# Optimization experiments

Measured on AMD Instinct MI355X. Metric: run time of the kernel, lower is better.

The kernel has to match this reference:

```python
import jax, jax.numpy as jnp
import numpy as np

N, K, M, C, OUT, S = 80000, 8, 1000, 128, 64, 2
EPS = 1e-5


def _bn(x, g, b, m, v):
    # eval-mode BatchNorm1d applied over the last (channel) axis
    return (x - m) * (g / jnp.sqrt(v + EPS)) + b


def setup_inputs() -> dict:
    key = jax.random.key(0)
    ks = jax.random.split(key, 40)
    it = iter(range(40))
    rn = lambda sh, s=1.0: jax.random.normal(ks[next(it)], sh, dtype=jnp.float32) * s
    ru = lambda sh: jax.random.uniform(ks[next(it)], sh, dtype=jnp.float32, minval=0.5, maxval=1.5)
    w = 0.05
    inp = {}
    inp["sp_fea"] = rn((M, C))
    inp["sp_xyz"] = rn((M, 3))
    inp["o_p_fea"] = rn((N, C))
    inp["p_xyz"] = rn((N, 3))
    # linear_q / linear_k / linear_v  (in_planes -> mid_planes)
    inp["Wq"] = rn((C, C), w); inp["bq"] = jnp.zeros((C,), jnp.float32)
    inp["Wk"] = rn((C, C), w); inp["bk"] = jnp.zeros((C,), jnp.float32)
    inp["Wv"] = rn((C, C), w); inp["bv"] = jnp.zeros((C,), jnp.float32)
    # linear_p: Linear(3,3) -> BN(3) -> ReLU -> Linear(3, mid)
    inp["Wp1"] = rn((3, 3), 0.5); inp["bp1"] = jnp.zeros((3,), jnp.float32)
    inp["gp"] = 1.0 + rn((3,), 0.1); inp["betap"] = rn((3,), 0.1)
    inp["mp"] = rn((3,), 0.1); inp["vp"] = ru((3,))
    inp["Wp2"] = rn((3, C), 0.3); inp["bp2"] = jnp.zeros((C,), jnp.float32)
    # linear_w: BN(mid) -> ReLU -> Linear(mid,out) -> BN(out) -> ReLU -> Linear(out,out)
    inp["g1"] = 1.0 + rn((C,), 0.1); inp["beta1"] = rn((C,), 0.1)
    inp["m1"] = rn((C,), 0.1); inp["v1"] = ru((C,))
    inp["W1"] = rn((C, OUT), w); inp["b1"] = jnp.zeros((OUT,), jnp.float32)
    inp["g2"] = 1.0 + rn((OUT,), 0.1); inp["beta2"] = rn((OUT,), 0.1)
    inp["m2"] = rn((OUT,), 0.1); inp["v2"] = ru((OUT,))
    inp["W2"] = rn((OUT, OUT), w); inp["b2"] = jnp.zeros((OUT,), jnp.float32)
    # index / offset inputs (ints)
    inp["c2p_idx_abs"] = jax.random.randint(ks[next(it)], (N, K), 0, M)
    inp["c2p_idx"] = jax.random.randint(ks[next(it)], (N, K), 0, M)
    inp["cluster_idx"] = jax.random.randint(ks[next(it)], (N,), 0, M)
    inp["offset"] = jnp.array([N], dtype=jnp.int32)
    inp["sp_offset"] = jnp.array([M], dtype=jnp.int32)
    return inp


def reference(sp_fea, sp_xyz, o_p_fea, p_xyz,
              Wq, bq, Wk, bk, Wv, bv,
              Wp1, bp1, gp, betap, mp, vp, Wp2, bp2,
              g1, beta1, m1, v1, W1, b1,
              g2, beta2, m2, v2, W2, b2,
              c2p_idx_abs, c2p_idx, cluster_idx, offset, sp_offset):
    q = o_p_fea @ Wq + bq                               # [N, C]
    k_sp = (sp_fea @ Wk + bk)[c2p_idx_abs]              # gather -> [N, K, C]
    v_sp = (sp_fea @ Wv + bv)[c2p_idx_abs]              # [N, K, C]
    p_e = sp_xyz[c2p_idx_abs]                           # [N, K, 3]
    # positional encoding MLP
    p_e = jax.nn.relu(_bn(p_e @ Wp1 + bp1, gp, betap, mp, vp)) @ Wp2 + bp2  # [N, K, C]
    # vector attention scores
    w = k_sp - q[:, None, :] + p_e                      # [N, K, C]
    w = jax.nn.relu(_bn(w, g1, beta1, m1, v1)) @ W1 + b1
    w = jax.nn.relu(_bn(w, g2, beta2, m2, v2)) @ W2 + b2  # [N, K, OUT]
    w = jax.nn.softmax(w, axis=1)                        # softmax over the K neighbors
    # shared-plane weighted sum
    bi = ((v_sp + p_e).reshape(N, K, S, C // S) * w[:, :, None, :]).reshape(N, K, C)
    bi = bi.sum(axis=2)                                  # [N, K]
    return jax.nn.softmax(bi, axis=1)                    # association matrix [N, K]
```

## Files before the change

### kernel.cpp

```cpp
#include <hip/hip_runtime.h>
#include <stdint.h>

#define EPS 1e-5f
#define LOG2E 1.4426950408889634f

#define NPTS 80000
#define CDIM 128
#define ODIM 64
#define KNBR 8
#define MSUP 1000

#define KP2H_OFF 0
#define UT_OFF   (256*1024)
#define WQF_OFF  (512*1024)
#define W1F_OFF  (544*1024)
#define W2F_OFF  (560*1024)
#define C1_OFF   (568*1024)
#define QSG_OFF  (576*1024)
#define WSTAGE_BYTES (16*1024 + 8*1024 + 256)

typedef float f32x4 __attribute__((ext_vector_type(4)));
typedef short bf16x8 __attribute__((ext_vector_type(8)));
typedef __bf16 bf16v8 __attribute__((ext_vector_type(8)));
typedef __bf16 bf16v4 __attribute__((ext_vector_type(4)));

union FragU { bf16x8 v; unsigned u[4]; uint4 q; };

#if __has_builtin(__builtin_amdgcn_cvt_pk_bf16_f32)
#define HAVE_PK_BF16 1
#endif

__device__ inline unsigned pk_bf16(float lo, float hi) {
#ifdef HAVE_PK_BF16
  typedef __bf16 bf16x2_t __attribute__((ext_vector_type(2)));
  return __builtin_bit_cast(unsigned, __builtin_amdgcn_cvt_pk_bf16_f32(lo, hi));
#else
  unsigned a = __builtin_bit_cast(unsigned, lo);
  unsigned b = __builtin_bit_cast(unsigned, hi);
  a += 0x7FFFu + ((a >> 16) & 1u);
  b += 0x7FFFu + ((b >> 16) & 1u);
  return (a >> 16) | (b & 0xFFFF0000u);
#endif
}

__device__ inline float exp2_fast(float x) {
#if __has_builtin(__builtin_amdgcn_exp2f)
  return __builtin_amdgcn_exp2f(x);
#else
  return exp2f(x);
#endif
}

__global__ __launch_bounds__(256)
void k_prep(const float* __restrict__ sp_fea, const float* __restrict__ sp_xyz,
            const float* __restrict__ Wk, const float* __restrict__ bk,
            const float* __restrict__ Wv, const float* __restrict__ bv,
            const float* __restrict__ Wp1, const float* __restrict__ bp1,
            const float* __restrict__ gp, const float* __restrict__ betap,
            const float* __restrict__ mp, const float* __restrict__ vp,
            const float* __restrict__ Wp2, const float* __restrict__ bp2,
            const float* __restrict__ g1, const float* __restrict__ beta1,
            const float* __restrict__ m1, const float* __restrict__ v1,
            const float* __restrict__ bq,
            const float* __restrict__ Wq, const float* __restrict__ W1,
            const float* __restrict__ W2,
            const float* __restrict__ g2, const float* __restrict__ v2,
            const float* __restrict__ b1, const float* __restrict__ m2,
            const float* __restrict__ beta2, char* __restrict__ ws)
{
  if (blockIdx.x < 1000) {
    unsigned short* kp2h = (unsigned short*)(ws + KP2H_OFF);
    float* uT = (float*)(ws + UT_OFF);
    const int m = blockIdx.x;
    const int t = threadIdx.x;
    const int c = t & 127, half = t >> 7;
    __shared__ float fea[128];
    __shared__ float pk[128], pv[128];
    if (t < 128) fea[t] = sp_fea[m * 128 + t];
    __syncthreads();
    float kv = 0.f, vv = 0.f;
    const float* wkc = Wk + half * 64 * 128 + c;
    const float* wvc = Wv + half * 64 * 128 + c;
    const float* feah = fea + half * 64;
    #pragma unroll 8
    for (int d = 0; d < 64; ++d) {
      const float f = feah[d];
      kv = fmaf(f, wkc[d * 128], kv);
      vv = fmaf(f, wvc[d * 128], vv);
    }
    if (half) { pk[c] = kv; pv[c] = vv; }
    __syncthreads();
    if (!half) {
      kv += pk[c] + bk[c];
      vv += pv[c] + bv[c];
      const float x0 = sp_xyz[m*3+0], x1 = sp_xyz[m*3+1], x2 = sp_xyz[m*3+2];
      float pe = bp2[c];
      #pragma unroll
      for (int ii = 0; ii < 3; ++ii) {
        float s = bp1[ii] + x0*Wp1[0*3+ii] + x1*Wp1[1*3+ii] + x2*Wp1[2*3+ii];
        s = (s - mp[ii]) * (gp[ii] * rsqrtf(vp[ii] + EPS)) + betap[ii];
        s = fmaxf(s, 0.0f);
        pe += s * Wp2[ii*128 + c];
      }
      const float s1c = g1[c] * rsqrtf(v1[c] + EPS);
      const float kpv = (kv + pe - m1[c] - bq[c]) * s1c + beta1[c];
      kp2h[m*128 + c] = (unsigned short)(pk_bf16(kpv, kpv) & 0xFFFFu);
      pv[c] = vv + pe;
    }
    __syncthreads();
    if (t < 64) uT[m*64 + t] = (pv[t] + pv[t + 64]) * LOG2E;
  } else {
    const int tid = (blockIdx.x - 1000) * 256 + threadIdx.x;
    if (tid < 2048) {
      const int e = tid, f = e >> 6, l = e & 63;
      const int kt = f >> 3, mt = f & 7;
      const int c = mt*16 + (l & 15);
      const int d0 = kt*32 + (l >> 4)*8;
      const float sc = g1[c] * rsqrtf(v1[c] + EPS);
      uint4 u;
      u.x = pk_bf16(Wq[(d0+0)*128 + c]*sc, Wq[(d0+1)*128 + c]*sc);
      u.y = pk_bf16(Wq[(d0+2)*128 + c]*sc, Wq[(d0+3)*128 + c]*sc);
      u.z = pk_bf16(Wq[(d0+4)*128 + c]*sc, Wq[(d0+5)*128 + c]*sc);
      u.w = pk_bf16(Wq[(d0+6)*128 + c]*sc, Wq[(d0+7)*128 + c]*sc);
      *(uint4*)(ws + WQF_OFF + e*16) = u;
    } else if (tid < 3072) {
      const int e = tid - 2048, f = e >> 6, l = e & 63;
      const int kt = f >> 2, jt = f & 3;
      const int j = jt*16 + (l & 15);
      const int c0 = kt*32 + (l >> 4)*8;
      const float sc = g2[j] * rsqrtf(v2[j] + EPS);
      uint4 u;
      u.x = pk_bf16(W1[(c0+0)*64 + j]*sc, W1[(c0+1)*64 + j]*sc);
      u.y = pk_bf16(W1[(c0+2)*64 + j]*sc, W1[(c0+3)*64 + j]*sc);
      u.z = pk_bf16(W1[(c0+4)*64 + j]*sc, W1[(c0+5)*64 + j]*sc);
      u.w = pk_bf16(W1[(c0+6)*64 + j]*sc, W1[(c0+7)*64 + j]*sc);
      *(uint4*)(ws + W1F_OFF + e*16) = u;
    } else if (tid < 3584) {
      const int e = tid - 3072, f = e >> 6, l = e & 63;
      const int kt2 = f >> 2, nt = f & 3;
      const int jp = nt*16 + (l & 15);
      const int j0 = kt2*32 + (l >> 4)*8;
      uint4 u;
      u.x = pk_bf16(W2[(j0+0)*64 + jp]*LOG2E, W2[(j0+1)*64 + jp]*LOG2E);
      u.y = pk_bf16(W2[(j0+2)*64 + jp]*LOG2E, W2[(j0+3)*64 + jp]*LOG2E);
      u.z = pk_bf16(W2[(j0+4)*64 + jp]*LOG2E, W2[(j0+5)*64 + jp]*LOG2E);
      u.w = pk_bf16(W2[(j0+6)*64 + jp]*LOG2E, W2[(j0+7)*64 + jp]*LOG2E);
      *(uint4*)(ws + W2F_OFF + e*16) = u;
    } else if (tid < 3648) {
      const int j = tid - 3584;
      const float sc = g2[j] * rsqrtf(v2[j] + EPS);
      ((float*)(ws + C1_OFF))[j] = (b1[j] - m2[j]) * sc + beta2[j];
    }
  }
}

__global__ __launch_bounds__(256, 4)
void k_q(const float* __restrict__ o_p_fea, char* __restrict__ ws)
{
  __shared__ __align__(16) char ldsq[32*1024];
  char* qs_g = ws + QSG_OFF;
  const int t = threadIdx.x;
  const int wave = t >> 6, l = t & 63;
  const int quad = l >> 4, row = l & 15;
  const int n0 = (blockIdx.x * 4 + wave) * 16;

  {
    const uint4* src = (const uint4*)(ws + WQF_OFF);
    uint4* dst = (uint4*)ldsq;
    #pragma unroll
    for (int i = 0; i < 8; ++i) dst[t + i*256] = src[t + i*256];
  }
  __syncthreads();

  f32x4 qa[8];
  #pragma unroll
  for (int mt = 0; mt < 8; ++mt) qa[mt] = (f32x4){0.f, 0.f, 0.f, 0.f};
  const float* feab = o_p_fea + (size_t)(n0 + row) * 128;
  #pragma unroll
  for (int kt = 0; kt < 4; ++kt) {
    f32x4 fa = *(const f32x4*)(feab + kt*32 + quad*8);
    f32x4 fb = *(const f32x4*)(feab + kt*32 + quad*8 + 4);
    FragU bu;
    bu.u[0] = pk_bf16(fa[0], fa[1]);
    bu.u[1] = pk_bf16(fa[2], fa[3]);
    bu.u[2] = pk_bf16(fb[0], fb[1]);
    bu.u[3] = pk_bf16(fb[2], fb[3]);
    #pragma unroll
    for (int mt = 0; mt < 8; ++mt) {
      const bf16x8 wf = *(const bf16x8*)(ldsq + ((kt*8+mt)*64 + l)*16);
      qa[mt] = __builtin_amdgcn_mfma_f32_16x16x32_bf16(wf, bu.v, qa[mt], 0, 0, 0);
    }
  }
  #pragma unroll
  for (int mt = 0; mt < 8; ++mt) {
    uint2 pp;
    pp.x = pk_bf16(qa[mt][0], qa[mt][1]);
    pp.y = pk_bf16(qa[mt][2], qa[mt][3]);
    *(uint2*)(qs_g + (size_t)(n0 + row) * 256 + mt*32 + quad*8) = pp;
  }
}

#define H2_PITCH 144
#define H2_SIZE  (16*144)
#define W1L_OFF  0
#define W2L_OFF  (16*1024)
#define C1L_OFF  (24*1024)
#define H2_BASE  24832
#define LDS_TOTAL (H2_BASE + 4*H2_SIZE)

__global__ __launch_bounds__(256, 3)
void k_main(const int* __restrict__ idx, const float* __restrict__ b2,
            const char* __restrict__ ws, float* __restrict__ out)
{
  const unsigned short* kp2h = (const unsigned short*)(ws + KP2H_OFF);
  const float* uT = (const float*)(ws + UT_OFF);
  const char* qs_g = ws + QSG_OFF;

  __shared__ __align__(16) char lds[LDS_TOTAL];
  const int t = threadIdx.x;
  const int wave = t >> 6, l = t & 63;
  const int quad = l >> 4, row = l & 15;
  char* h2_w = lds + H2_BASE + wave * H2_SIZE;

  const int slot = blockIdx.x * 4 + wave;
  const int gid0 = slot * 4;
  const int nloc = row >> 3;

  {
    const uint4* src = (const uint4*)(ws + W1F_OFF);
    uint4* dst = (uint4*)lds;
    #pragma unroll
    for (int i = 0; i < 7; ++i) {
      const int e = t + i * 256;
      if (e < WSTAGE_BYTES / 16) dst[e] = src[e];
    }
  }

  int mr4[4];
  #pragma unroll
  for (int g = 0; g < 4; ++g) mr4[g] = idx[(gid0 + g)*16 + row];

  __syncthreads();

  f32x4 c1r[4];
  #pragma unroll
  for (int jt = 0; jt < 4; ++jt)
    c1r[jt] = *(const f32x4*)(lds + C1L_OFF + (jt*16 + quad*4)*4);
  float b2r[4];
  #pragma unroll
  for (int nt = 0; nt < 4; ++nt) b2r[nt] = b2[row + nt*16] * LOG2E;

  int msc[4];
  #pragma unroll
  for (int rg = 0; rg < 4; ++rg) msc[rg] = idx[gid0*16 + quad*4 + rg];
  uint4 kfc[4], qpc[4];
  {
    const uint4* kr = (const uint4*)(kp2h + (size_t)mr4[0] * 128);
    const uint4* qr = (const uint4*)(qs_g + (size_t)(gid0*2 + nloc) * 256);
    #pragma unroll
    for (int kt = 0; kt < 4; ++kt) { kfc[kt] = kr[kt*4 + quad]; qpc[kt] = qr[kt*4 + quad]; }
  }

  #pragma unroll 1
  for (int g = 0; g < 4; ++g) {
    const int gid = gid0 + g;
    int msn[4];
    uint4 kfn[4], qpn[4];
    if (g < 3) {
      #pragma unroll
      for (int rg = 0; rg < 4; ++rg) msn[rg] = idx[(gid+1)*16 + quad*4 + rg];
      const uint4* kr = (const uint4*)(kp2h + (size_t)mr4[g+1] * 128);
      const uint4* qr = (const uint4*)(qs_g + (size_t)((gid+1)*2 + nloc) * 256);
      #pragma unroll
      for (int kt = 0; kt < 4; ++kt) { kfn[kt] = kr[kt*4 + quad]; qpn[kt] = qr[kt*4 + quad]; }
    }
    float u4[4][4];
    #pragma unroll
    for (int rg = 0; rg < 4; ++rg) {
      const float* ur = uT + (size_t)msc[rg] * 64 + row;
      #pragma unroll
      for (int nt = 0; nt < 4; ++nt) u4[rg][nt] = ur[nt*16];
    }

    f32x4 a1[4];
    #pragma unroll
    for (int jt = 0; jt < 4; ++jt) a1[jt] = (f32x4){0.f, 0.f, 0.f, 0.f};
    #pragma unroll
    for (int kt = 0; kt < 4; ++kt) {
      const bf16v8 kv = __builtin_bit_cast(bf16v8, kfc[kt]);
      const bf16v8 qv = __builtin_bit_cast(bf16v8, qpc[kt]);
      bf16v8 z = {};
      bf16v8 x = __builtin_elementwise_max((bf16v8)(kv - qv), z);
      FragU xf;
      xf.q = __builtin_bit_cast(uint4, x);
      #pragma unroll
      for (int jt = 0; jt < 4; ++jt) {
        const bf16x8 wf = *(const bf16x8*)(lds + W1L_OFF + (kt*4+jt)*1024 + l*16);
        a1[jt] = __builtin_amdgcn_mfma_f32_16x16x32_bf16(wf, xf.v, a1[jt], 0, 0, 0);
      }
    }

    #pragma unroll
    for (int jt = 0; jt < 4; ++jt) {
      f32x4 v = a1[jt] + c1r[jt];
      uint2 pp;
      pp.x = pk_bf16(v[0], v[1]);
      pp.y = pk_bf16(v[2], v[3]);
      bf16v4 h = __builtin_bit_cast(bf16v4, pp);
      bf16v4 z4 = {};
      h = __builtin_elementwise_max(h, z4);
      pp = __builtin_bit_cast(uint2, h);
      *(uint2*)(h2_w + row*H2_PITCH + (jt*16 + quad*4)*2) = pp;
    }

    f32x4 a2[4];
    #pragma unroll
    for (int nt = 0; nt < 4; ++nt) a2[nt] = (f32x4){0.f, 0.f, 0.f, 0.f};
    #pragma unroll
    for (int kt2 = 0; kt2 < 2; ++kt2) {
      const bf16x8 af = *(const bf16x8*)(h2_w + row*H2_PITCH + kt2*64 + quad*16);
      #pragma unroll
      for (int nt = 0; nt < 4; ++nt) {
        const bf16x8 wf = *(const bf16x8*)(lds + W2L_OFF + (kt2*4+nt)*1024 + l*16);
        a2[nt] = __builtin_amdgcn_mfma_f32_16x16x32_bf16(af, wf, a2[nt], 0, 0, 0);
      }
    }
    float e[4][4], rs[4];
    #pragma unroll
    for (int nt = 0; nt < 4; ++nt) {
      #pragma unroll
      for (int rg = 0; rg < 4; ++rg) e[nt][rg] = exp2_fast(a2[nt][rg] + b2r[nt]);
      float s = e[nt][0] + e[nt][1] + e[nt][2] + e[nt][3];
      s += __shfl_xor(s, 16);
      rs[nt] = __builtin_amdgcn_rcpf(s);
    }
    float bi[4] = {0.f, 0.f, 0.f, 0.f};
    #pragma unroll
    for (int rg = 0; rg < 4; ++rg) {
      #pragma unroll
      for (int nt = 0; nt < 4; ++nt)
        bi[rg] = fmaf(e[nt][rg] * rs[nt], u4[rg][nt], bi[rg]);
    }
    #pragma unroll
    for (int rg = 0; rg < 4; ++rg) {
      float b = bi[rg];
      b += __shfl_xor(b, 1);
      b += __shfl_xor(b, 2);
      b += __shfl_xor(b, 4);
      b += __shfl_xor(b, 8);
      bi[rg] = b;
    }
    const float eb0 = exp2_fast(bi[0]), eb1 = exp2_fast(bi[1]);
    const float eb2 = exp2_fast(bi[2]), eb3 = exp2_fast(bi[3]);
    float sb = eb0 + eb1 + eb2 + eb3;
    sb += __shfl_xor(sb, 16);
    const float rsb = __builtin_amdgcn_rcpf(sb);
    if (row < 4) {
      const float vsel = row == 0 ? eb0 : row == 1 ? eb1 : row == 2 ? eb2 : eb3;
      out[gid*16 + quad*4 + row] = vsel * rsb;
    }
    if (g < 3) {
      #pragma unroll
      for (int rg = 0; rg < 4; ++rg) msc[rg] = msn[rg];
      #pragma unroll
      for (int kt = 0; kt < 4; ++kt) { kfc[kt] = kfn[kt]; qpc[kt] = qpn[kt]; }
    }
  }
}

extern "C" void kernel_launch(void* const* d_in, const int* in_sizes, int n_in,
                              void* d_out, int out_size, void* d_ws, size_t ws_size,
                              hipStream_t stream)
{
  const float* sp_fea  = (const float*)d_in[0];
  const float* sp_xyz  = (const float*)d_in[1];
  const float* o_p_fea = (const float*)d_in[2];
  const float* Wq    = (const float*)d_in[4];
  const float* bq    = (const float*)d_in[5];
  const float* Wk    = (const float*)d_in[6];
  const float* bk    = (const float*)d_in[7];
  const float* Wv    = (const float*)d_in[8];
  const float* bv    = (const float*)d_in[9];
  const float* Wp1   = (const float*)d_in[10];
  const float* bp1   = (const float*)d_in[11];
  const float* gp    = (const float*)d_in[12];
  const float* betap = (const float*)d_in[13];
  const float* mp    = (const float*)d_in[14];
  const float* vp    = (const float*)d_in[15];
  const float* Wp2   = (const float*)d_in[16];
  const float* bp2   = (const float*)d_in[17];
  const float* g1    = (const float*)d_in[18];
  const float* beta1 = (const float*)d_in[19];
  const float* m1    = (const float*)d_in[20];
  const float* v1    = (const float*)d_in[21];
  const float* W1    = (const float*)d_in[22];
  const float* b1    = (const float*)d_in[23];
  const float* g2    = (const float*)d_in[24];
  const float* beta2 = (const float*)d_in[25];
  const float* m2    = (const float*)d_in[26];
  const float* v2    = (const float*)d_in[27];
  const float* W2    = (const float*)d_in[28];
  const float* b2    = (const float*)d_in[29];
  const int* c2p_idx_abs = (const int*)d_in[30];

  char* ws = (char*)d_ws;
  float* out = (float*)d_out;

  hipLaunchKernelGGL(k_prep, dim3(1015), dim3(256), 0, stream,
                     sp_fea, sp_xyz, Wk, bk, Wv, bv, Wp1, bp1, gp, betap, mp, vp,
                     Wp2, bp2, g1, beta1, m1, v1, bq,
                     Wq, W1, W2, g2, v2, b1, m2, beta2, ws);
  hipLaunchKernelGGL(k_q, dim3(1250), dim3(256), 0, stream,
                     o_p_fea, ws);
  hipLaunchKernelGGL(k_main, dim3(2500), dim3(256), 0, stream,
                     c2p_idx_abs, b2, ws, out);
}
```

Baseline: 214.7 us.

## Software-pipeline softmax epilogue one group behind the MFMA stages

Moves the softmax and weighted-sum epilogue into a helper that runs on the previous group's saved MFMA accumulators and u values. Each epilogue can then be scheduled alongside the current group's matrix work, with a final drain after the loop. The aim is to hide the exp, shuffle and reciprocal latency behind MFMA. The cost is higher register pressure from the carried state under launch_bounds(256,3), which may cause spills. The first iteration also runs a wasted epilogue on zeros with its store masked off.

```diff
diff --git a/kernel.cpp b/kernel.cpp
--- a/kernel.cpp
+++ b/kernel.cpp
@@ -208,6 +208,49 @@
 #define H2_BASE  24832
 #define LDS_TOTAL (H2_BASE + 4*H2_SIZE)
 
+struct EpiState { f32x4 a2[4]; float u4[4][4]; };
+
+__device__ __forceinline__ void epilogue(const EpiState& st, const float* b2r,
+                                         int quad, int row,
+                                         float* __restrict__ out, int base,
+                                         bool wr)
+{
+  float e[4][4], rs[4];
+  #pragma unroll
+  for (int nt = 0; nt < 4; ++nt) {
+    #pragma unroll
+    for (int rg = 0; rg < 4; ++rg) e[nt][rg] = exp2_fast(st.a2[nt][rg] + b2r[nt]);
+    float s = e[nt][0] + e[nt][1] + e[nt][2] + e[nt][3];
+    s += __shfl_xor(s, 16);
+    rs[nt] = __builtin_amdgcn_rcpf(s);
+  }
+  float bi[4] = {0.f, 0.f, 0.f, 0.f};
+  #pragma unroll
+  for (int rg = 0; rg < 4; ++rg) {
+    #pragma unroll
+    for (int nt = 0; nt < 4; ++nt)
+      bi[rg] = fmaf(e[nt][rg] * rs[nt], st.u4[rg][nt], bi[rg]);
+  }
+  #pragma unroll
+  for (int rg = 0; rg < 4; ++rg) {
+    float b = bi[rg];
+    b += __shfl_xor(b, 1);
+    b += __shfl_xor(b, 2);
+    b += __shfl_xor(b, 4);
+    b += __shfl_xor(b, 8);
+    bi[rg] = b;
+  }
+  const float eb0 = exp2_fast(bi[0]), eb1 = exp2_fast(bi[1]);
+  const float eb2 = exp2_fast(bi[2]), eb3 = exp2_fast(bi[3]);
+  float sb = eb0 + eb1 + eb2 + eb3;
+  sb += __shfl_xor(sb, 16);
+  const float rsb = __builtin_amdgcn_rcpf(sb);
+  if (wr && row < 4) {
+    const float vsel = row == 0 ? eb0 : row == 1 ? eb1 : row == 2 ? eb2 : eb3;
+    out[base + quad*4 + row] = vsel * rsb;
+  }
+}
+
 __global__ __launch_bounds__(256, 3)
 void k_main(const int* __restrict__ idx, const float* __restrict__ b2,
             const char* __restrict__ ws, float* __restrict__ out)
@@ -261,6 +304,14 @@
     for (int kt = 0; kt < 4; ++kt) { kfc[kt] = kr[kt*4 + quad]; qpc[kt] = qr[kt*4 + quad]; }
   }
 
+  EpiState st;
+  #pragma unroll
+  for (int nt = 0; nt < 4; ++nt) {
+    st.a2[nt] = (f32x4){0.f, 0.f, 0.f, 0.f};
+    #pragma unroll
+    for (int rg = 0; rg < 4; ++rg) st.u4[nt][rg] = 0.f;
+  }
+
   #pragma unroll 1
   for (int g = 0; g < 4; ++g) {
     const int gid = gid0 + g;
@@ -274,12 +325,12 @@
       #pragma unroll
       for (int kt = 0; kt < 4; ++kt) { kfn[kt] = kr[kt*4 + quad]; qpn[kt] = qr[kt*4 + quad]; }
     }
-    float u4[4][4];
+    float u4n[4][4];
     #pragma unroll
     for (int rg = 0; rg < 4; ++rg) {
       const float* ur = uT + (size_t)msc[rg] * 64 + row;
       #pragma unroll
-      for (int nt = 0; nt < 4; ++nt) u4[rg][nt] = ur[nt*16];
+      for (int nt = 0; nt < 4; ++nt) u4n[rg][nt] = ur[nt*16];
     }
 
     f32x4 a1[4];
@@ -325,40 +376,19 @@
         a2[nt] = __builtin_amdgcn_mfma_f32_16x16x32_bf16(af, wf, a2[nt], 0, 0, 0);
       }
     }
-    float e[4][4], rs[4];
-    #pragma unroll
-    for (int nt = 0; nt < 4; ++nt) {
-      #pragma unroll
-      for (int rg = 0; rg < 4; ++rg) e[nt][rg] = exp2_fast(a2[nt][rg] + b2r[nt]);
-      float s = e[nt][0] + e[nt][1] + e[nt][2] + e[nt][3];
-      s += __shfl_xor(s, 16);
-      rs[nt] = __builtin_amdgcn_rcpf(s);
-    }
-    float bi[4] = {0.f, 0.f, 0.f, 0.f};
-    #pragma unroll
-    for (int rg = 0; rg < 4; ++rg) {
-      #pragma unroll
-      for (int nt = 0; nt < 4; ++nt)
-        bi[rg] = fmaf(e[nt][rg] * rs[nt], u4[rg][nt], bi[rg]);
-    }
-    #pragma unroll
-    for (int rg = 0; rg < 4; ++rg) {
-      float b = bi[rg];
-      b += __shfl_xor(b, 1);
-      b += __shfl_xor(b, 2);
-      b += __shfl_xor(b, 4);
-      b += __shfl_xor(b, 8);
-      bi[rg] = b;
-    }
-    const float eb0 = exp2_fast(bi[0]), eb1 = exp2_fast(bi[1]);
-    const float eb2 = exp2_fast(bi[2]), eb3 = exp2_fast(bi[3]);
-    float sb = eb0 + eb1 + eb2 + eb3;
-    sb += __shfl_xor(sb, 16);
-    const float rsb = __builtin_amdgcn_rcpf(sb);
-    if (row < 4) {
-      const float vsel = row == 0 ? eb0 : row == 1 ? eb1 : row == 2 ? eb2 : eb3;
-      out[gid*16 + quad*4 + row] = vsel * rsb;
-    }
+
+    {
+      const int gm1 = gid - 1;
+      const int base = (gm1 < gid0 ? gid0 : gm1) * 16;
+      epilogue(st, b2r, quad, row, out, base, g > 0);
+    }
+
+    #pragma unroll
+    for (int nt = 0; nt < 4; ++nt) st.a2[nt] = a2[nt];
+    #pragma unroll
+    for (int rg = 0; rg < 4; ++rg)
+      #pragma unroll
+      for (int nt = 0; nt < 4; ++nt) st.u4[rg][nt] = u4n[rg][nt];
     if (g < 3) {
       #pragma unroll
       for (int rg = 0; rg < 4; ++rg) msc[rg] = msn[rg];
@@ -366,6 +396,7 @@
       for (int kt = 0; kt < 4; ++kt) { kfc[kt] = kfn[kt]; qpc[kt] = qpn[kt]; }
     }
   }
+  epilogue(st, b2r, quad, row, out, (gid0 + 3) * 16, true);
 }
 
 extern "C" void kernel_launch(void* const* d_in, const int* in_sizes, int n_in,
```

Result: slower. 279.0 us (+29.9%).
